# Optimization experiments

Hardware: AMD Instinct MI355X
Metric: run time of the kernel (lower is better)

The kernel has to match this reference:

```python
import jax, jax.numpy as jnp
import numpy as np

HEAD_SIZE = 256
HEAD_SIZE_R = HEAD_SIZE // 4   # 64, RoPE slice
HEAD_SIZE_C = HEAD_SIZE - HEAD_SIZE_R  # 192
N_EMBD = 256


def rope(x, start_pos=0):
    # x: [B, T, d_r] with interleaved (even, odd) pairs
    B, T, d = x.shape
    half = d // 2
    theta = 1.0 / (10000.0 ** (jnp.arange(half, dtype=x.dtype) / half))  # [half]
    idx = jnp.arange(start_pos, start_pos + T, dtype=x.dtype)[:, None] * theta[None, :]  # [T, half]
    sin, cos = jnp.sin(idx), jnp.cos(idx)
    xs = x.reshape(B, T, half, 2)
    x1, x2 = xs[..., 0], xs[..., 1]
    rot = jnp.stack([x1 * cos - x2 * sin, x1 * sin + x2 * cos], axis=-1)
    return rot.reshape(B, T, d)


def setup_inputs() -> dict:
    key = jax.random.key(0)
    ks = jax.random.split(key, 8)
    B, T = 32, 2048
    s = 0.05
    return {
        "x": jax.random.normal(ks[0], (B, T, N_EMBD), dtype=jnp.float32),
        "Wq_comp": jax.random.normal(ks[1], (N_EMBD, N_EMBD), dtype=jnp.float32) * s,
        "Wkv_comp": jax.random.normal(ks[2], (N_EMBD, N_EMBD), dtype=jnp.float32) * s,
        "Wqc": jax.random.normal(ks[3], (N_EMBD, HEAD_SIZE_C), dtype=jnp.float32) * s,
        "Wqr": jax.random.normal(ks[4], (N_EMBD, HEAD_SIZE_R), dtype=jnp.float32) * s,
        "Wkc": jax.random.normal(ks[5], (N_EMBD, HEAD_SIZE_C), dtype=jnp.float32) * s,
        "Wkr": jax.random.normal(ks[6], (N_EMBD, HEAD_SIZE_R), dtype=jnp.float32) * s,
        "Wv": jax.random.normal(ks[7], (N_EMBD, HEAD_SIZE), dtype=jnp.float32) * s,
    }


def reference(x, Wq_comp, Wkv_comp, Wqc, Wqr, Wkc, Wkr, Wv):
    # Low-rank compression
    c_q = x @ Wq_comp      # [B,T,C]
    c_kv = x @ Wkv_comp    # [B,T,C]
    # Q: content + rotary slice
    q_c = c_q @ Wqc                      # [B,T,192]
    q_r = rope(c_q @ Wqr, start_pos=0)   # [B,T,64]
    q = jnp.concatenate([q_c, q_r], axis=-1)  # [B,T,256]
    # K: content + rotary slice
    k_c = c_kv @ Wkc
    k_r = rope(c_kv @ Wkr, start_pos=0)
    k = jnp.concatenate([k_c, k_r], axis=-1)  # [B,T,256]
    v = c_kv @ Wv                              # [B,T,256]
    # Causal attention (dropout is identity in eval)
    scale = 1.0 / jnp.sqrt(jnp.asarray(HEAD_SIZE, dtype=x.dtype))
    wei = jnp.einsum('bqd,bkd->bqk', q, k) * scale  # [B,T,T]
    T_q = q.shape[1]
    mask = jnp.tril(jnp.ones((T_q, T_q), dtype=bool))
    wei = jnp.where(mask, wei, jnp.asarray(-jnp.inf, dtype=wei.dtype))
    wei = jax.nn.softmax(wei, axis=-1)
    out = jnp.einsum('bqk,bkd->bqd', wei, v)  # [B,T,256]
    return out, (k, v)
```

## Files before the change

kernel.cpp:

```cpp
#include <hip/hip_runtime.h>

typedef float  f32x4  __attribute__((ext_vector_type(4)));
typedef __bf16 bf16x8 __attribute__((ext_vector_type(8)));
typedef unsigned short u16x8 __attribute__((ext_vector_type(8)));
typedef unsigned short u16x4 __attribute__((ext_vector_type(4)));

#define DEV static __device__ __forceinline__

DEV unsigned short f2b(float f) {
  unsigned int u = __float_as_uint(f);
  u += 0x7fffu + ((u >> 16) & 1u);
  return (unsigned short)(u >> 16);
}
DEV float b2f(unsigned short h) { return __uint_as_float(((unsigned int)h) << 16); }

DEV f32x4 mfma16(bf16x8 a, bf16x8 b, f32x4 c) {
  return __builtin_amdgcn_mfma_f32_16x16x32_bf16(a, b, c, 0, 0, 0);
}

__global__ __launch_bounds__(256) void k_prep(
    const float* __restrict__ Wq_comp, const float* __restrict__ Wkv_comp,
    const float* __restrict__ Wqc, const float* __restrict__ Wqr,
    const float* __restrict__ Wkc, const float* __restrict__ Wkr,
    const float* __restrict__ Wv,
    unsigned short* __restrict__ W1t, unsigned short* __restrict__ Wqt,
    unsigned short* __restrict__ Wkvt, float* __restrict__ ct, float* __restrict__ st) {
  int tid = blockIdx.x * 256 + threadIdx.x;
  if (tid < 131072) {
    int n = tid >> 8, k = tid & 255;
    float v = (n < 256) ? Wq_comp[k * 256 + n] : Wkv_comp[k * 256 + (n - 256)];
    W1t[tid] = f2b(v);
  } else if (tid < 196608) {
    int t2 = tid - 131072; int n = t2 >> 8, k = t2 & 255;
    float v = (n < 192) ? Wqc[k * 192 + n] : Wqr[k * 64 + (n - 192)];
    Wqt[t2] = f2b(v);
  } else if (tid < 327680) {
    int t2 = tid - 196608; int n = t2 >> 8, k = t2 & 255;
    float v = (n < 192) ? Wkc[k * 192 + n]
             : (n < 256) ? Wkr[k * 64 + (n - 192)] : Wv[k * 256 + (n - 256)];
    Wkvt[t2] = f2b(v);
  } else if (tid < 393216) {
    int t2 = tid - 327680; int t = t2 >> 5, i = t2 & 31;
    float theta = powf(10000.0f, -(float)i / 32.0f);
    float ang = (float)t * theta;
    ct[t2] = cosf(ang); st[t2] = sinf(ang);
  }
}

__global__ __launch_bounds__(512, 2) void k_gemm1(const float* __restrict__ X,
    const unsigned short* __restrict__ Bt, unsigned short* __restrict__ Cq,
    unsigned short* __restrict__ Ckv) {
  __shared__ __align__(16) unsigned short Ash[128 * 72];
  __shared__ __align__(16) unsigned short Bsh[256 * 72];
  const int nt2 = blockIdx.x, mt = blockIdx.y;
  const int tid = threadIdx.x;
  const int l = tid & 63, wv = tid >> 6, li = l & 15, g = l >> 4;
  const int wm = wv >> 2, wn = wv & 3;
  const f32x4 zf = {0.f, 0.f, 0.f, 0.f};
  f32x4 acc[4][4];
#pragma unroll
  for (int i = 0; i < 4; ++i)
#pragma unroll
    for (int j = 0; j < 4; ++j) acc[i][j] = zf;
  for (int kb = 0; kb < 256; kb += 64) {
    __syncthreads();
#pragma unroll
    for (int it = 0; it < 4; ++it) {
      int idx = it * 512 + tid;
      int row = idx >> 4, c4 = (idx & 15) << 2;
      f32x4 v = *reinterpret_cast<const f32x4*>(X + (size_t)(mt * 128 + row) * 256 + kb + c4);
      u16x4 u = { f2b(v.x), f2b(v.y), f2b(v.z), f2b(v.w) };
      *reinterpret_cast<u16x4*>(&Ash[row * 72 + c4]) = u;
    }
#pragma unroll
    for (int it = 0; it < 4; ++it) {
      int idx = it * 512 + tid;
      int row = idx >> 3, c8 = (idx & 7) << 3;
      *reinterpret_cast<u16x8*>(&Bsh[row * 72 + c8]) =
        *reinterpret_cast<const u16x8*>(Bt + (size_t)(nt2 * 256 + row) * 256 + kb + c8);
    }
    __syncthreads();
#pragma unroll
    for (int kc = 0; kc < 2; ++kc) {
      bf16x8 a[4], b[4];
#pragma unroll
      for (int mf = 0; mf < 4; ++mf)
        a[mf] = *reinterpret_cast<const bf16x8*>(&Ash[(wm * 64 + mf * 16 + li) * 72 + kc * 32 + g * 8]);
#pragma unroll
      for (int nf = 0; nf < 4; ++nf)
        b[nf] = *reinterpret_cast<const bf16x8*>(&Bsh[(wn * 64 + nf * 16 + li) * 72 + kc * 32 + g * 8]);
#pragma unroll
      for (int mf = 0; mf < 4; ++mf)
#pragma unroll
        for (int nf = 0; nf < 4; ++nf)
          acc[mf][nf] = mfma16(a[mf], b[nf], acc[mf][nf]);
    }
  }
  unsigned short* C = nt2 ? Ckv : Cq;
#pragma unroll
  for (int mf = 0; mf < 4; ++mf)
#pragma unroll
    for (int nf = 0; nf < 4; ++nf)
#pragma unroll
      for (int r = 0; r < 4; ++r) {
        int row = mt * 128 + wm * 64 + mf * 16 + g * 4 + r;
        int col = wn * 64 + nf * 16 + li;
        C[(size_t)row * 256 + col] = f2b(acc[mf][nf][r]);
      }
}

__global__ __launch_bounds__(512, 2) void k_gemm2(const unsigned short* __restrict__ Cq,
    const unsigned short* __restrict__ Ckv,
    const unsigned short* __restrict__ Wqt, const unsigned short* __restrict__ Wkvt,
    unsigned short* __restrict__ q_ws, unsigned short* __restrict__ k_ws,
    float* __restrict__ kout, float* __restrict__ vout,
    unsigned short* __restrict__ vt,
    const float* __restrict__ ct, const float* __restrict__ st, int sel0) {
  __shared__ __align__(16) unsigned short Ash[128 * 72];
  __shared__ __align__(16) unsigned short Bsh[256 * 72];
  const int sel = sel0 + blockIdx.x, mt = blockIdx.y;
  const int tid = threadIdx.x;
  const int l = tid & 63, wv = tid >> 6, li = l & 15, g = l >> 4;
  const int wm = wv >> 2, wn = wv & 3;
  const unsigned short* Asrc = (sel == 0) ? Cq : Ckv;
  const unsigned short* Wt = (sel == 0) ? Wqt : Wkvt;
  const int wrow = (sel == 2) ? 256 : 0;
  const f32x4 zf = {0.f, 0.f, 0.f, 0.f};
  f32x4 acc[4][4];
#pragma unroll
  for (int i = 0; i < 4; ++i)
#pragma unroll
    for (int j = 0; j < 4; ++j) acc[i][j] = zf;
  for (int kb = 0; kb < 256; kb += 64) {
    __syncthreads();
#pragma unroll
    for (int it = 0; it < 2; ++it) {
      int idx = it * 512 + tid;
      int row = idx >> 3, c8 = (idx & 7) << 3;
      *reinterpret_cast<u16x8*>(&Ash[row * 72 + c8]) =
        *reinterpret_cast<const u16x8*>(Asrc + (size_t)(mt * 128 + row) * 256 + kb + c8);
    }
#pragma unroll
    for (int it = 0; it < 4; ++it) {
      int idx = it * 512 + tid;
      int row = idx >> 3, c8 = (idx & 7) << 3;
      *reinterpret_cast<u16x8*>(&Bsh[row * 72 + c8]) =
        *reinterpret_cast<const u16x8*>(Wt + (size_t)(wrow + row) * 256 + kb + c8);
    }
    __syncthreads();
#pragma unroll
    for (int kc = 0; kc < 2; ++kc) {
      bf16x8 a[4], b[4];
#pragma unroll
      for (int mf = 0; mf < 4; ++mf)
        a[mf] = *reinterpret_cast<const bf16x8*>(&Ash[(wm * 64 + mf * 16 + li) * 72 + kc * 32 + g * 8]);
#pragma unroll
      for (int nf = 0; nf < 4; ++nf)
        b[nf] = *reinterpret_cast<const bf16x8*>(&Bsh[(wn * 64 + nf * 16 + li) * 72 + kc * 32 + g * 8]);
#pragma unroll
      for (int mf = 0; mf < 4; ++mf)
#pragma unroll
        for (int nf = 0; nf < 4; ++nf)
          acc[mf][nf] = mfma16(a[mf], b[nf], acc[mf][nf]);
    }
  }
  if (sel < 2 && wn == 3) {
#pragma unroll
    for (int mf = 0; mf < 4; ++mf)
#pragma unroll
      for (int nf = 0; nf < 4; ++nf)
#pragma unroll
        for (int r = 0; r < 4; ++r) {
          float v = acc[mf][nf][r];
          float other = __shfl_xor(v, 1);
          int t = (mt * 128 + wm * 64 + mf * 16 + g * 4 + r) & 2047;
          int i = nf * 8 + (li >> 1);
          float c = ct[t * 32 + i], s = st[t * 32 + i];
          acc[mf][nf][r] = (li & 1) ? (other * s + v * c) : (v * c - other * s);
        }
  }
#pragma unroll
  for (int mf = 0; mf < 4; ++mf)
#pragma unroll
    for (int nf = 0; nf < 4; ++nf) {
      int cl = wn * 64 + nf * 16 + li;
#pragma unroll
      for (int r = 0; r < 4; ++r) {
        int row = mt * 128 + wm * 64 + mf * 16 + g * 4 + r;
        float val = acc[mf][nf][r];
        if (sel == 0) {
          q_ws[(size_t)row * 256 + cl] = f2b(val);
        } else if (sel == 1) {
          k_ws[(size_t)row * 256 + cl] = f2b(val);
          kout[(size_t)row * 256 + cl] = val;
        } else {
          vout[(size_t)row * 256 + cl] = val;
        }
      }
    }
  if (sel == 2) {
    const int batch = mt >> 4, tbase = (mt & 15) * 128;
#pragma unroll
    for (int h = 0; h < 2; ++h) {
      __syncthreads();
      if (wm == h) {
#pragma unroll
        for (int mf = 0; mf < 4; ++mf)
#pragma unroll
          for (int nf = 0; nf < 4; ++nf)
#pragma unroll
            for (int r = 0; r < 4; ++r) {
              int lr = mf * 16 + g * 4 + r;
              int col = wn * 64 + nf * 16 + li;
              Bsh[lr * 258 + col] = f2b(acc[mf][nf][r]);
            }
      }
      __syncthreads();
#pragma unroll
      for (int it2 = 0; it2 < 8; ++it2) {
        int idx = it2 * 512 + tid;
        int d = idx >> 4, tq = (idx & 15) << 2;
        u16x4 pk = { Bsh[(tq + 0) * 258 + d], Bsh[(tq + 1) * 258 + d],
                     Bsh[(tq + 2) * 258 + d], Bsh[(tq + 3) * 258 + d] };
        *reinterpret_cast<u16x4*>(vt + ((size_t)batch * 256 + d) * 2048 + tbase + h * 64 + tq) = pk;
      }
    }
  }
}

__global__ __launch_bounds__(256, 2) void k_attn(
    const unsigned short* __restrict__ q_ws, const unsigned short* __restrict__ k_ws,
    const unsigned short* __restrict__ vt_ws, float* __restrict__ out) {
  __shared__ __align__(16) unsigned short Ksh[64 * 256];
  __shared__ __align__(16) unsigned short Vsh[256 * 64];
  __shared__ __align__(16) unsigned short Psh[4][1024];
  const int b = blockIdx.x;
  const int qt = 31 - (int)blockIdx.y;
  const int tid = threadIdx.x;
  const int l = tid & 63, wv = tid >> 6, li = l & 15, g = l >> 4;
  const f32x4 zf = {0.f, 0.f, 0.f, 0.f};
  const float C1 = 0.09016844005556021f;
  const float C2 = -11.541560327111707f;

  u16x8 ones_u = {0x3F80, 0x3F80, 0x3F80, 0x3F80, 0x3F80, 0x3F80, 0x3F80, 0x3F80};
  bf16x8 ones = *reinterpret_cast<bf16x8*>(&ones_u);

  const unsigned short* kbase = k_ws + (size_t)b * 2048 * 256;
  const unsigned short* vbase = vt_ws + (size_t)b * 256 * 2048;

  u16x8 kreg[8], vreg[8];
#define LOADREGS(t)                                                                   \
  {                                                                                   \
    const unsigned short* ks_ = kbase + (size_t)(t) * 64 * 256;                       \
    const unsigned short* vs_ = vbase + (size_t)(t) * 64;                             \
    _Pragma("unroll")                                                                 \
    for (int rnd = 0; rnd < 8; ++rnd) {                                               \
      int chunk = rnd * 256 + tid;                                                    \
      kreg[rnd] = *reinterpret_cast<const u16x8*>(ks_ + (size_t)(chunk >> 5) * 256 + (chunk & 31) * 8); \
    }                                                                                 \
    _Pragma("unroll")                                                                 \
    for (int rnd = 0; rnd < 8; ++rnd) {                                               \
      int chunk = rnd * 256 + tid;                                                    \
      vreg[rnd] = *reinterpret_cast<const u16x8*>(vs_ + (size_t)(chunk >> 3) * 2048 + (chunk & 7) * 8); \
    }                                                                                 \
  }

  const int wq0 = qt * 64 + wv * 16;
  bf16x8 qf[8];
  const unsigned short* qp = q_ws + ((size_t)b * 2048 + wq0 + li) * 256;
#pragma unroll
  for (int kc = 0; kc < 8; ++kc)
    qf[kc] = *reinterpret_cast<const bf16x8*>(qp + kc * 32 + g * 8);

  f32x4 o[16];
#pragma unroll
  for (int i = 0; i < 16; ++i) o[i] = zf;
  f32x4 ol = zf;

  const int nj = qt + 1;
  LOADREGS(0);

  for (int j = 0; j < nj; ++j) {
    __syncthreads();
#pragma unroll
    for (int rnd = 0; rnd < 8; ++rnd) {
      int chunk = rnd * 256 + tid;
      int row = chunk >> 5, pc = chunk & 31;
      *reinterpret_cast<u16x8*>(&Ksh[row * 256 + (pc ^ (row & 7)) * 8]) = kreg[rnd];
    }
#pragma unroll
    for (int rnd = 0; rnd < 8; ++rnd) {
      int chunk = rnd * 256 + tid;
      int d = chunk >> 3, pc = chunk & 7;
      *reinterpret_cast<u16x8*>(&Vsh[d * 64 + (pc ^ (d & 7)) * 8]) = vreg[rnd];
    }
    __syncthreads();
    if (j + 1 < nj) LOADREGS(j + 1);

    f32x4 s[4];
#pragma unroll
    for (int nf = 0; nf < 4; ++nf) s[nf] = zf;
#pragma unroll
    for (int kc = 0; kc < 8; ++kc) {
      int pc = (kc * 4 + g) ^ (li & 7);
#pragma unroll
      for (int nf = 0; nf < 4; ++nf) {
        bf16x8 bk = *reinterpret_cast<const bf16x8*>(&Ksh[(nf * 16 + li) * 256 + pc * 8]);
        s[nf] = mfma16(qf[kc], bk, s[nf]);
      }
    }
    const bool diag = (j == qt);
#pragma unroll
    for (int r = 0; r < 4; ++r) {
      const int q = g * 4 + r;
#pragma unroll
      for (int nf = 0; nf < 4; ++nf) {
        float pv = __builtin_amdgcn_exp2f(__builtin_fmaf(s[nf][r], C1, C2));
        if (diag && (j * 64 + nf * 16 + li) > (wq0 + q)) pv = 0.f;
        int kk = nf * 16 + li;
        int pcp = (kk >> 3) ^ (q & 7);
        Psh[wv][q * 64 + pcp * 8 + (kk & 7)] =
            (unsigned short)(__float_as_uint(pv) >> 16);
      }
    }
#pragma unroll
    for (int kc2 = 0; kc2 < 2; ++kc2) {
      int pcp = (kc2 * 4 + g) ^ (li & 7);
      bf16x8 pa = *reinterpret_cast<const bf16x8*>(&Psh[wv][li * 64 + pcp * 8]);
      ol = mfma16(pa, ones, ol);
#pragma unroll
      for (int nfd = 0; nfd < 16; ++nfd) {
        int d = nfd * 16 + li;
        bf16x8 bv = *reinterpret_cast<const bf16x8*>(&Vsh[d * 64 + pcp * 8]);
        o[nfd] = mfma16(pa, bv, o[nfd]);
      }
    }
  }

#pragma unroll
  for (int r = 0; r < 4; ++r) {
    float inv = 1.0f / ol[r];
    int qrow = wq0 + g * 4 + r;
    float* op = out + ((size_t)b * 2048 + qrow) * 256;
#pragma unroll
    for (int nfd = 0; nfd < 16; ++nfd)
      op[nfd * 16 + li] = o[nfd][r] * inv;
  }
#undef LOADREGS
}

extern "C" void kernel_launch(void* const* d_in, const int* in_sizes, int n_in,
                              void* d_out, int out_size, void* d_ws, size_t ws_size,
                              hipStream_t stream) {
  const float* x        = (const float*)d_in[0];
  const float* Wq_comp  = (const float*)d_in[1];
  const float* Wkv_comp = (const float*)d_in[2];
  const float* Wqc      = (const float*)d_in[3];
  const float* Wqr      = (const float*)d_in[4];
  const float* Wkc      = (const float*)d_in[5];
  const float* Wkr      = (const float*)d_in[6];
  const float* Wv       = (const float*)d_in[7];

  float* out  = (float*)d_out;
  float* kout = out + 16777216;
  float* vout = out + 33554432;

  if (ws_size < 135397376u) return;

  char* ws = (char*)d_ws;
  unsigned short* c_q  = (unsigned short*)(ws);
  unsigned short* vt   = (unsigned short*)(ws);
  unsigned short* c_kv = (unsigned short*)(ws + 33554432);
  unsigned short* q_ws = (unsigned short*)(ws + 67108864);
  unsigned short* k_ws = (unsigned short*)(ws + 100663296);
  unsigned short* W1t  = (unsigned short*)(ws + 134217728);
  unsigned short* Wqt  = W1t + 131072;
  unsigned short* Wkvt = Wqt + 65536;
  float* ct = (float*)(Wkvt + 131072);
  float* st = ct + 65536;

  k_prep<<<1536, 256, 0, stream>>>(Wq_comp, Wkv_comp, Wqc, Wqr, Wkc, Wkr, Wv,
                                   W1t, Wqt, Wkvt, ct, st);
  k_gemm1<<<dim3(2, 512), 512, 0, stream>>>(x, W1t, c_q, c_kv);
  k_gemm2<<<dim3(2, 512), 512, 0, stream>>>(c_q, c_kv, Wqt, Wkvt, q_ws, k_ws,
                                            kout, vout, vt, ct, st, 0);
  k_gemm2<<<dim3(1, 512), 512, 0, stream>>>(c_q, c_kv, Wqt, Wkvt, q_ws, k_ws,
                                            kout, vout, vt, ct, st, 2);
  k_attn<<<dim3(32, 32), 256, 0, stream>>>(q_ws, k_ws, vt, out);
}
```

Baseline: 313.2 us.

## Enlarge attention query tile to 128 rows with 8 waves sharing K/V tiles

The attention kernel now uses 512-thread blocks covering 128 query rows, so each K/V tile staged in shared memory is reused by eight waves instead of four, halving global K/V traffic per query. Waves skip key tiles lying wholly above their causal diagonal. The P tile is handled in two 32-key halves with a smaller per-wave buffer and a new swizzle. Query tiles are dispatched in an interleaved order to balance causal work. The trade-offs are fewer blocks in the grid, idle waves near the diagonal, and a launch bound of four waves per SIMD that may constrain registers for the 16 accumulator vectors.

```diff
diff --git a/kernel.cpp b/kernel.cpp
--- a/kernel.cpp
+++ b/kernel.cpp
@@ -228,14 +228,15 @@
   }
 }
 
-__global__ __launch_bounds__(256, 2) void k_attn(
+__global__ __launch_bounds__(512, 4) void k_attn(
     const unsigned short* __restrict__ q_ws, const unsigned short* __restrict__ k_ws,
     const unsigned short* __restrict__ vt_ws, float* __restrict__ out) {
   __shared__ __align__(16) unsigned short Ksh[64 * 256];
   __shared__ __align__(16) unsigned short Vsh[256 * 64];
-  __shared__ __align__(16) unsigned short Psh[4][1024];
+  __shared__ __align__(16) unsigned short Psh[8][512];
   const int b = blockIdx.x;
-  const int qt = 31 - (int)blockIdx.y;
+  const int yy = blockIdx.y;
+  const int qt = (yy < 8) ? (15 - 2 * yy) : (2 * (yy - 8));
   const int tid = threadIdx.x;
   const int l = tid & 63, wv = tid >> 6, li = l & 15, g = l >> 4;
   const f32x4 zf = {0.f, 0.f, 0.f, 0.f};
@@ -248,24 +249,24 @@
   const unsigned short* kbase = k_ws + (size_t)b * 2048 * 256;
   const unsigned short* vbase = vt_ws + (size_t)b * 256 * 2048;
 
-  u16x8 kreg[8], vreg[8];
+  u16x8 kreg[4], vreg[4];
 #define LOADREGS(t)                                                                   \
   {                                                                                   \
     const unsigned short* ks_ = kbase + (size_t)(t) * 64 * 256;                       \
     const unsigned short* vs_ = vbase + (size_t)(t) * 64;                             \
     _Pragma("unroll")                                                                 \
-    for (int rnd = 0; rnd < 8; ++rnd) {                                               \
-      int chunk = rnd * 256 + tid;                                                    \
+    for (int rnd = 0; rnd < 4; ++rnd) {                                               \
+      int chunk = rnd * 512 + tid;                                                    \
       kreg[rnd] = *reinterpret_cast<const u16x8*>(ks_ + (size_t)(chunk >> 5) * 256 + (chunk & 31) * 8); \
     }                                                                                 \
     _Pragma("unroll")                                                                 \
-    for (int rnd = 0; rnd < 8; ++rnd) {                                               \
-      int chunk = rnd * 256 + tid;                                                    \
+    for (int rnd = 0; rnd < 4; ++rnd) {                                               \
+      int chunk = rnd * 512 + tid;                                                    \
       vreg[rnd] = *reinterpret_cast<const u16x8*>(vs_ + (size_t)(chunk >> 3) * 2048 + (chunk & 7) * 8); \
     }                                                                                 \
   }
 
-  const int wq0 = qt * 64 + wv * 16;
+  const int wq0 = qt * 128 + wv * 16;
   bf16x8 qf[8];
   const unsigned short* qp = q_ws + ((size_t)b * 2048 + wq0 + li) * 256;
 #pragma unroll
@@ -277,62 +278,69 @@
   for (int i = 0; i < 16; ++i) o[i] = zf;
   f32x4 ol = zf;
 
-  const int nj = qt + 1;
+  const int nj = 2 * qt + 2;
   LOADREGS(0);
 
   for (int j = 0; j < nj; ++j) {
     __syncthreads();
 #pragma unroll
-    for (int rnd = 0; rnd < 8; ++rnd) {
-      int chunk = rnd * 256 + tid;
+    for (int rnd = 0; rnd < 4; ++rnd) {
+      int chunk = rnd * 512 + tid;
       int row = chunk >> 5, pc = chunk & 31;
       *reinterpret_cast<u16x8*>(&Ksh[row * 256 + (pc ^ (row & 7)) * 8]) = kreg[rnd];
     }
 #pragma unroll
-    for (int rnd = 0; rnd < 8; ++rnd) {
-      int chunk = rnd * 256 + tid;
+    for (int rnd = 0; rnd < 4; ++rnd) {
+      int chunk = rnd * 512 + tid;
       int d = chunk >> 3, pc = chunk & 7;
       *reinterpret_cast<u16x8*>(&Vsh[d * 64 + (pc ^ (d & 7)) * 8]) = vreg[rnd];
     }
     __syncthreads();
     if (j + 1 < nj) LOADREGS(j + 1);
 
-    f32x4 s[4];
-#pragma unroll
-    for (int nf = 0; nf < 4; ++nf) s[nf] = zf;
-#pragma unroll
-    for (int kc = 0; kc < 8; ++kc) {
-      int pc = (kc * 4 + g) ^ (li & 7);
-#pragma unroll
-      for (int nf = 0; nf < 4; ++nf) {
-        bf16x8 bk = *reinterpret_cast<const bf16x8*>(&Ksh[(nf * 16 + li) * 256 + pc * 8]);
-        s[nf] = mfma16(qf[kc], bk, s[nf]);
-      }
-    }
-    const bool diag = (j == qt);
-#pragma unroll
-    for (int r = 0; r < 4; ++r) {
-      const int q = g * 4 + r;
-#pragma unroll
-      for (int nf = 0; nf < 4; ++nf) {
-        float pv = __builtin_amdgcn_exp2f(__builtin_fmaf(s[nf][r], C1, C2));
-        if (diag && (j * 64 + nf * 16 + li) > (wq0 + q)) pv = 0.f;
-        int kk = nf * 16 + li;
-        int pcp = (kk >> 3) ^ (q & 7);
-        Psh[wv][q * 64 + pcp * 8 + (kk & 7)] =
-            (unsigned short)(__float_as_uint(pv) >> 16);
-      }
-    }
-#pragma unroll
-    for (int kc2 = 0; kc2 < 2; ++kc2) {
-      int pcp = (kc2 * 4 + g) ^ (li & 7);
-      bf16x8 pa = *reinterpret_cast<const bf16x8*>(&Psh[wv][li * 64 + pcp * 8]);
-      ol = mfma16(pa, ones, ol);
-#pragma unroll
-      for (int nfd = 0; nfd < 16; ++nfd) {
-        int d = nfd * 16 + li;
-        bf16x8 bv = *reinterpret_cast<const bf16x8*>(&Vsh[d * 64 + pcp * 8]);
-        o[nfd] = mfma16(pa, bv, o[nfd]);
+    if (j * 64 <= wq0 + 15) {
+      f32x4 s[4];
+#pragma unroll
+      for (int nf = 0; nf < 4; ++nf) s[nf] = zf;
+#pragma unroll
+      for (int kc = 0; kc < 8; ++kc) {
+        int pc = (kc * 4 + g) ^ (li & 7);
+#pragma unroll
+        for (int nf = 0; nf < 4; ++nf) {
+          bf16x8 bk = *reinterpret_cast<const bf16x8*>(&Ksh[(nf * 16 + li) * 256 + pc * 8]);
+          s[nf] = mfma16(qf[kc], bk, s[nf]);
+        }
+      }
+      const bool needmask = (j * 64 + 63) > wq0;
+#pragma unroll
+      for (int h = 0; h < 2; ++h) {
+#pragma unroll
+        for (int r = 0; r < 4; ++r) {
+          const int q = g * 4 + r;
+          const int sw = (q & 3) ^ (q >> 2);
+#pragma unroll
+          for (int nf2 = 0; nf2 < 2; ++nf2) {
+            const int nf = h * 2 + nf2;
+            float pv = __builtin_amdgcn_exp2f(__builtin_fmaf(s[nf][r], C1, C2));
+            if (needmask) {
+              int kg = j * 64 + nf * 16 + li;
+              if (kg > wq0 + q) pv = 0.f;
+            }
+            int kkl = nf2 * 16 + li;
+            Psh[wv][q * 32 + (((kkl >> 3) ^ sw) << 3) + (kkl & 7)] =
+                (unsigned short)(__float_as_uint(pv) >> 16);
+          }
+        }
+        bf16x8 pa = *reinterpret_cast<const bf16x8*>(
+            &Psh[wv][li * 32 + ((g ^ (li & 3) ^ (li >> 2)) << 3)]);
+        ol = mfma16(pa, ones, ol);
+        const int cb = h * 4 + g;
+#pragma unroll
+        for (int nfd = 0; nfd < 16; ++nfd) {
+          int d = nfd * 16 + li;
+          bf16x8 bv = *reinterpret_cast<const bf16x8*>(&Vsh[d * 64 + (cb ^ (d & 7)) * 8]);
+          o[nfd] = mfma16(pa, bv, o[nfd]);
+        }
       }
     }
   }
@@ -386,5 +394,5 @@
                                             kout, vout, vt, ct, st, 0);
   k_gemm2<<<dim3(1, 512), 512, 0, stream>>>(c_q, c_kv, Wqt, Wkvt, q_ws, k_ws,
                                             kout, vout, vt, ct, st, 2);
-  k_attn<<<dim3(32, 32), 256, 0, stream>>>(q_ws, k_ws, vt, out);
-}
+  k_attn<<<dim3(32, 16), 512, 0, stream>>>(q_ws, k_ws, vt, out);
+}
```

New measurement: 593.8 us. 89.6% more time.
